# Performance work log

Hardware: AMD Instinct MI355X
Metric: run time of the kernel (lower is better)

## Reference

```python
import jax, jax.numpy as jnp
import numpy as np

EPS = 1e-5  # BatchNorm eps (eval mode, running stats mean=0, var=1)
BN_SCALE = 1.0 / np.sqrt(1.0 + EPS)


def setup_inputs() -> dict:
    key = jax.random.key(0)
    ks = jax.random.split(key, 5)
    N, T, C, V, K = 64, 300, 64, 25, 3
    x = jax.random.normal(ks[0], (N, T, C, V), dtype=jnp.float32)
    # G: Linear(T -> 2T, no bias), Linear(2T -> K, no bias)
    g_w1 = jax.random.normal(ks[1], (2 * T, T), dtype=jnp.float32) * (1.0 / np.sqrt(T))
    g_w2 = jax.random.normal(ks[2], (K, 2 * T), dtype=jnp.float32) * (1.0 / np.sqrt(2 * T))
    # L: Conv1d(C -> C//4, K, pad=K//2, no bias), Conv1d(C//4 -> C, 1, no bias)
    l_w1 = jax.random.normal(ks[3], (C // 4, C, K), dtype=jnp.float32) * (1.0 / np.sqrt(C * K))
    l_w2 = jax.random.normal(ks[4], (C, C // 4), dtype=jnp.float32) * (1.0 / np.sqrt(C // 4))
    return {"x": x, "g_w1": g_w1, "g_w2": g_w2, "l_w1": l_w1, "l_w2": l_w2}


def reference(x, g_w1, g_w2, l_w1, l_w2):
    # x: [N, T, C, V]; n_segment == T so n_batch == N
    N, T, C, V = x.shape
    K = g_w2.shape[0]
    pad = K // 2
    # new_x: [N, C, T, V]
    new_x = jnp.transpose(x, (0, 2, 1, 3))
    # adaptive avg pool over V -> [N, C, T]
    pooled = jnp.mean(new_x, axis=-1)

    # --- G branch: per-(n,c) temporal kernel of size K ---
    g_in = pooled.reshape(N * C, T)                         # [N*C, T]
    h = jnp.maximum(g_in @ g_w1.T * BN_SCALE, 0.0)          # Linear + BN(eval) + ReLU
    conv_kernel = jax.nn.softmax(h @ g_w2.T, axis=-1)       # [N*C, K]
    conv_kernel = conv_kernel.reshape(N, C, K)

    # --- L branch: local activation over time ---
    z = jax.lax.conv_general_dilated(
        pooled, l_w1, window_strides=(1,), padding=[(pad, pad)],
        dimension_numbers=("NCH", "OIH", "NCH"))              # [N, C//4, T]
    z = jnp.maximum(z * BN_SCALE, 0.0)
    local_act = jax.nn.sigmoid(jnp.einsum("nct,oc->not", z, l_w2))  # [N, C, T]

    new_x = new_x * local_act[..., None]                    # [N, C, T, V]

    # --- per-(n,c) depthwise temporal conv (groups = N*C) ---
    xpad = jnp.pad(new_x, ((0, 0), (0, 0), (pad, pad), (0, 0)))
    windows = jnp.stack([xpad[:, :, k:k + T, :] for k in range(K)], axis=-1)  # [N,C,T,V,K]
    out = jnp.einsum("nctvk,nck->nctv", windows, conv_kernel)

    return jnp.transpose(out, (0, 2, 1, 3))                 # [N, T, C, V]
```

## Files before the change

### kernel.cpp

```cpp
#include <hip/hip_runtime.h>
#include <math.h>

#define BN_SCALE_F 0.99999500003749969f


__global__ __launch_bounds__(256) void pool_prep_kernel(const float* __restrict__ x,
                                                        const float* __restrict__ g_w1,
                                                        const float* __restrict__ l_w1,
                                                        float* __restrict__ pooled,
                                                        float* __restrict__ w1p,
                                                        float* __restrict__ lw1r) {
  __shared__ float buf[6400];
  int bid = blockIdx.x;
  if (bid < 4800) {
    const float4* src = (const float4*)(x + (size_t)bid * 6400);
    float4* b4 = (float4*)buf;
    for (int i = threadIdx.x; i < 1600; i += 256) b4[i] = src[i];
    __syncthreads();
    int wave = threadIdx.x >> 6;
    int c = threadIdx.x & 63;
    int nt = bid * 4 + wave;
    int n = nt / 300, t = nt - n * 300;
    const float* p = buf + wave * 1600 + c * 25;
    float s = 0.f;
#pragma unroll
    for (int v = 0; v < 25; ++v) s += p[v];
    pooled[((size_t)(n * 64 + c)) * 300 + t] = s * 0.04f;
  } else if (bid < 4850) {
    int b = bid - 4800;
    float* tile = buf;
    int tj = b % 10, tk = b / 10;
    int j0 = tj * 64, k0 = tk * 64;
    for (int it = 0; it < 16; ++it) {
      int i = threadIdx.x + it * 256;
      int jj = i >> 6, kk = i & 63;
      int j = j0 + jj, k = k0 + kk;
      tile[jj * 65 + kk] = (j < 600 && k < 300) ? g_w1[(size_t)j * 300 + k] : 0.f;
    }
    __syncthreads();
    for (int it = 0; it < 16; ++it) {
      int jloc = threadIdx.x >> 2;
      int kkm = threadIdx.x & 3;
      int kloc = it * 4 + kkm;
      int j = j0 + jloc, k = k0 + kloc;
      if (j < 600 && k < 300) {
        w1p[(size_t)(k >> 2) * 2400 + (size_t)j * 4 + (k & 3)] = tile[jloc * 65 + kloc];
      }
    }
  } else {
    for (int i = threadIdx.x; i < 3072; i += 256) {
      int o = i / 192;
      int rem = i - o * 192;
      int c = rem / 3;
      int k = rem - c * 3;
      lw1r[c * 48 + o * 3 + k] = l_w1[i];
    }
  }
}

union GLSmem {
  struct {
    float rows[8][300];
    float wsum[5][24];
  } g;
  struct {
    float p[64][80];
    float z[75][20];
  } l;
};

__global__ __launch_bounds__(320) void gl_kernel(const float* __restrict__ pooled,
                                                 const float* __restrict__ w1p,
                                                 const float* __restrict__ g_w2,
                                                 const float* __restrict__ lw1r,
                                                 const float* __restrict__ l_w2,
                                                 float* __restrict__ kern,
                                                 float* __restrict__ la) {
  __shared__ GLSmem sm;
  int bid = blockIdx.x;
  int tid = threadIdx.x;
  if (bid < 512) {
    int r0 = bid * 8;
    {
      const float4* src = (const float4*)(pooled + (size_t)r0 * 300);
      float4* dst = (float4*)&sm.g.rows[0][0];
      for (int i = tid; i < 600; i += 320) dst[i] = src[i];
    }
    __syncthreads();

    int j1 = tid;
    int j2 = tid + 320;
    bool has2 = (j2 < 600);
    int j2c = has2 ? j2 : j1;
    const float4* wp = (const float4*)w1p;

    float acc1[8], acc2[8];
#pragma unroll
    for (int r = 0; r < 8; ++r) { acc1[r] = 0.f; acc2[r] = 0.f; }

    float4 wa = wp[j1];
    float4 wb = wp[j2c];
    for (int k4 = 0; k4 < 75; ++k4) {
      float4 wan, wbn;
      if (k4 < 74) {
        wan = wp[(size_t)(k4 + 1) * 600 + j1];
        wbn = wp[(size_t)(k4 + 1) * 600 + j2c];
      } else {
        wan = wa;
        wbn = wb;
      }
#pragma unroll
      for (int r = 0; r < 8; ++r) {
        float4 rv = *(const float4*)(&sm.g.rows[r][k4 * 4]);
        acc1[r] = fmaf(rv.x, wa.x, acc1[r]);
        acc1[r] = fmaf(rv.y, wa.y, acc1[r]);
        acc1[r] = fmaf(rv.z, wa.z, acc1[r]);
        acc1[r] = fmaf(rv.w, wa.w, acc1[r]);
        acc2[r] = fmaf(rv.x, wb.x, acc2[r]);
        acc2[r] = fmaf(rv.y, wb.y, acc2[r]);
        acc2[r] = fmaf(rv.z, wb.z, acc2[r]);
        acc2[r] = fmaf(rv.w, wb.w, acc2[r]);
      }
      wa = wan;
      wb = wbn;
    }

    float w2a0 = g_w2[j1], w2a1 = g_w2[600 + j1], w2a2 = g_w2[1200 + j1];
    float w2b0 = g_w2[j2c], w2b1 = g_w2[600 + j2c], w2b2 = g_w2[1200 + j2c];

    float lacc[24];
#pragma unroll
    for (int r = 0; r < 8; ++r) {
      float h1 = fmaxf(acc1[r] * BN_SCALE_F, 0.f);
      float h2 = has2 ? fmaxf(acc2[r] * BN_SCALE_F, 0.f) : 0.f;
      lacc[r * 3 + 0] = fmaf(h1, w2a0, h2 * w2b0);
      lacc[r * 3 + 1] = fmaf(h1, w2a1, h2 * w2b1);
      lacc[r * 3 + 2] = fmaf(h1, w2a2, h2 * w2b2);
    }

#pragma unroll
    for (int off = 1; off < 64; off <<= 1) {
#pragma unroll
      for (int i = 0; i < 24; ++i) lacc[i] += __shfl_xor(lacc[i], off, 64);
    }
    int wave = tid >> 6;
    int lane = tid & 63;
    if (lane == 0) {
#pragma unroll
      for (int i = 0; i < 24; ++i) sm.g.wsum[wave][i] = lacc[i];
    }
    __syncthreads();
    if (wave == 0) {
      float s = 0.f;
      if (lane < 24) {
#pragma unroll
        for (int w = 0; w < 5; ++w) s += sm.g.wsum[w][lane];
      }
      float a = __shfl(s, lane * 3 + 0, 64);
      float b = __shfl(s, lane * 3 + 1, 64);
      float c = __shfl(s, lane * 3 + 2, 64);
      if (lane < 8) {
        float m = fmaxf(a, fmaxf(b, c));
        float ea = expf(a - m), eb = expf(b - m), ec = expf(c - m);
        float inv = 1.f / (ea + eb + ec);
        size_t o = (size_t)(r0 + lane) * 3;
        kern[o] = ea * inv;
        kern[o + 1] = eb * inv;
        kern[o + 2] = ec * inv;
      }
    }
  } else {
    int bid2 = bid - 512;
    int n = bid2 >> 2;
    int tc = bid2 & 3;
    int t0 = tc * 75;
    for (int i = tid; i < 64 * 77; i += 320) {
      int c = i / 77, tt = i - c * 77;
      int gt = t0 - 1 + tt;
      sm.l.p[c][tt] = (gt >= 0 && gt < 300) ? pooled[(size_t)(n * 64 + c) * 300 + gt] : 0.f;
    }
    __syncthreads();
    {
      int og = tid / 80;
      int tl = tid - og * 80;
      if (tl < 75) {
        float acc[4] = {0.f, 0.f, 0.f, 0.f};
        for (int c = 0; c < 64; ++c) {
          const float* wr = lw1r + c * 48 + og * 12;
          float pk0 = sm.l.p[c][tl];
          float pk1 = sm.l.p[c][tl + 1];
          float pk2 = sm.l.p[c][tl + 2];
#pragma unroll
          for (int oi = 0; oi < 4; ++oi) {
            acc[oi] = fmaf(wr[oi * 3 + 0], pk0, acc[oi]);
            acc[oi] = fmaf(wr[oi * 3 + 1], pk1, acc[oi]);
            acc[oi] = fmaf(wr[oi * 3 + 2], pk2, acc[oi]);
          }
        }
        float4 zv;
        zv.x = fmaxf(acc[0] * BN_SCALE_F, 0.f);
        zv.y = fmaxf(acc[1] * BN_SCALE_F, 0.f);
        zv.z = fmaxf(acc[2] * BN_SCALE_F, 0.f);
        zv.w = fmaxf(acc[3] * BN_SCALE_F, 0.f);
        *(float4*)(&sm.l.z[tl][og * 4]) = zv;
      }
    }
    __syncthreads();
    {
      int c = tid / 5;
      int ts = tid - c * 5;
      const float4* w2v = (const float4*)(l_w2 + c * 16);
      float4 wA = w2v[0], wB = w2v[1], wC = w2v[2], wD = w2v[3];
      float* outp = la + (size_t)(n * 64 + c) * 300 + t0;
      for (int it = 0; it < 15; ++it) {
        int tl = ts + it * 5;
        const float4* zv = (const float4*)(&sm.l.z[tl][0]);
        float4 zA = zv[0], zB = zv[1], zC = zv[2], zD = zv[3];
        float s = zA.x * wA.x + zA.y * wA.y + zA.z * wA.z + zA.w * wA.w;
        s += zB.x * wB.x + zB.y * wB.y + zB.z * wB.z + zB.w * wB.w;
        s += zC.x * wC.x + zC.y * wC.y + zC.z * wC.z + zC.w * wC.w;
        s += zD.x * wD.x + zD.y * wD.y + zD.z * wD.z + zD.w * wD.w;
        outp[tl] = 1.f / (1.f + expf(-s));
      }
    }
  }
}

__global__ __launch_bounds__(256) void tam_final_kernel(const float* __restrict__ x,
                                                        const float* __restrict__ la,
                                                        const float* __restrict__ kern,
                                                        float* __restrict__ out) {
  int bid = blockIdx.x;
  int n = bid >> 4;
  int rem = bid & 15;
  int tch = rem >> 1;
  int half = rem & 1;
  int cv4 = half * 256 + threadIdx.x;
  if (cv4 >= 400) return;
  int e0 = cv4 * 4;
  int c0 = e0 / 25;
  int c3 = (e0 + 3) / 25;
  bool s1 = ((e0 + 1) / 25) != c0;
  bool s2 = ((e0 + 2) / 25) != c0;
  bool s3 = (c3 != c0);
  const float* lap0 = la + (size_t)(n * 64 + c0) * 300;
  const float* lap1 = la + (size_t)(n * 64 + c3) * 300;
  const float* kp0 = kern + (size_t)(n * 64 + c0) * 3;
  const float* kp1 = kern + (size_t)(n * 64 + c3) * 3;
  float k00 = kp0[0], k01 = kp0[1], k02 = kp0[2];
  float k10 = kp1[0], k11 = kp1[1], k12 = kp1[2];
  float4 K0 = {k00, s1 ? k10 : k00, s2 ? k10 : k00, s3 ? k10 : k00};
  float4 K1 = {k01, s1 ? k11 : k01, s2 ? k11 : k01, s3 ? k11 : k01};
  float4 K2 = {k02, s1 ? k12 : k02, s2 ? k12 : k02, s3 ? k12 : k02};

  const float4* xp = (const float4*)(x + (size_t)n * 480000) + cv4;
  float4* op = (float4*)(out + (size_t)n * 480000) + cv4;

  int t0 = tch * 38;
  int tend = t0 + 38;
  if (tend > 300) tend = 300;

#define LAMUL(dst, t)                                        \
  {                                                          \
    float l0 = lap0[(t)];                                    \
    float l1 = lap1[(t)];                                    \
    float4 xv = xp[(size_t)(t) * 400];                       \
    dst.x = xv.x * l0;                                       \
    dst.y = xv.y * (s1 ? l1 : l0);                           \
    dst.z = xv.z * (s2 ? l1 : l0);                           \
    dst.w = xv.w * (s3 ? l1 : l0);                           \
  }

  float4 am, ac, an;
  if (t0 > 0) {
    LAMUL(am, t0 - 1);
  } else {
    am = {0.f, 0.f, 0.f, 0.f};
  }
  LAMUL(ac, t0);
  for (int t = t0; t < tend; ++t) {
    if (t + 1 < 300) {
      LAMUL(an, t + 1);
    } else {
      an = {0.f, 0.f, 0.f, 0.f};
    }
    float4 o;
    o.x = fmaf(am.x, K0.x, fmaf(ac.x, K1.x, an.x * K2.x));
    o.y = fmaf(am.y, K0.y, fmaf(ac.y, K1.y, an.y * K2.y));
    o.z = fmaf(am.z, K0.z, fmaf(ac.z, K1.z, an.z * K2.z));
    o.w = fmaf(am.w, K0.w, fmaf(ac.w, K1.w, an.w * K2.w));
    op[(size_t)t * 400] = o;
    am = ac;
    ac = an;
  }
#undef LAMUL
}

extern "C" void kernel_launch(void* const* d_in, const int* in_sizes, int n_in,
                              void* d_out, int out_size, void* d_ws, size_t ws_size,
                              hipStream_t stream) {
  const float* x = (const float*)d_in[0];
  const float* g_w1 = (const float*)d_in[1];
  const float* g_w2 = (const float*)d_in[2];
  const float* l_w1 = (const float*)d_in[3];
  const float* l_w2 = (const float*)d_in[4];
  float* out = (float*)d_out;
  float* ws = (float*)d_ws;
  float* pooled = ws;
  float* kern = ws + 1228800;
  float* lact = ws + 1228800 + 12288;
  float* w1p = ws + 1228800 + 12288 + 1228800;
  float* lw1r = w1p + 180000;

  hipLaunchKernelGGL(pool_prep_kernel, dim3(4851), dim3(256), 0, stream, x, g_w1, l_w1,
                     pooled, w1p, lw1r);
  hipLaunchKernelGGL(gl_kernel, dim3(768), dim3(320), 0, stream, pooled, w1p, g_w2,
                     lw1r, l_w2, kern, lact);
  hipLaunchKernelGGL(tam_final_kernel, dim3(1024), dim3(256), 0, stream, x, lact, kern, out);
}
```

Before: 122.2 us.

## Register-tile G-branch GEMM with 4 outputs per thread and LDS-staged second layer

Reworks the G-branch first Linear so 150 threads each compute 4 hidden units times 8 rows, raising register reuse of the LDS row reads. Hidden activations are written to shared memory, and the second Linear is computed per (row,k) logit by one wave reduction each, replacing the 24-value butterfly shuffle reduction across all threads. The cost is that only 150 of 320 threads do the main GEMM, a larger shared-memory footprint, and an extra barrier.

```diff
diff --git a/kernel.cpp b/kernel.cpp
--- a/kernel.cpp
+++ b/kernel.cpp
@@ -61,7 +61,8 @@
 union GLSmem {
   struct {
     float rows[8][300];
-    float wsum[5][24];
+    float hbuf[8][600];
+    float logits[24];
   } g;
   struct {
     float p[64][80];
@@ -88,86 +89,68 @@
     }
     __syncthreads();
 
-    int j1 = tid;
-    int j2 = tid + 320;
-    bool has2 = (j2 < 600);
-    int j2c = has2 ? j2 : j1;
-    const float4* wp = (const float4*)w1p;
-
-    float acc1[8], acc2[8];
-#pragma unroll
-    for (int r = 0; r < 8; ++r) { acc1[r] = 0.f; acc2[r] = 0.f; }
-
-    float4 wa = wp[j1];
-    float4 wb = wp[j2c];
-    for (int k4 = 0; k4 < 75; ++k4) {
-      float4 wan, wbn;
-      if (k4 < 74) {
-        wan = wp[(size_t)(k4 + 1) * 600 + j1];
-        wbn = wp[(size_t)(k4 + 1) * 600 + j2c];
-      } else {
-        wan = wa;
-        wbn = wb;
-      }
-#pragma unroll
-      for (int r = 0; r < 8; ++r) {
-        float4 rv = *(const float4*)(&sm.g.rows[r][k4 * 4]);
-        acc1[r] = fmaf(rv.x, wa.x, acc1[r]);
-        acc1[r] = fmaf(rv.y, wa.y, acc1[r]);
-        acc1[r] = fmaf(rv.z, wa.z, acc1[r]);
-        acc1[r] = fmaf(rv.w, wa.w, acc1[r]);
-        acc2[r] = fmaf(rv.x, wb.x, acc2[r]);
-        acc2[r] = fmaf(rv.y, wb.y, acc2[r]);
-        acc2[r] = fmaf(rv.z, wb.z, acc2[r]);
-        acc2[r] = fmaf(rv.w, wb.w, acc2[r]);
-      }
-      wa = wan;
-      wb = wbn;
-    }
-
-    float w2a0 = g_w2[j1], w2a1 = g_w2[600 + j1], w2a2 = g_w2[1200 + j1];
-    float w2b0 = g_w2[j2c], w2b1 = g_w2[600 + j2c], w2b2 = g_w2[1200 + j2c];
-
-    float lacc[24];
-#pragma unroll
-    for (int r = 0; r < 8; ++r) {
-      float h1 = fmaxf(acc1[r] * BN_SCALE_F, 0.f);
-      float h2 = has2 ? fmaxf(acc2[r] * BN_SCALE_F, 0.f) : 0.f;
-      lacc[r * 3 + 0] = fmaf(h1, w2a0, h2 * w2b0);
-      lacc[r * 3 + 1] = fmaf(h1, w2a1, h2 * w2b1);
-      lacc[r * 3 + 2] = fmaf(h1, w2a2, h2 * w2b2);
-    }
-
-#pragma unroll
-    for (int off = 1; off < 64; off <<= 1) {
-#pragma unroll
-      for (int i = 0; i < 24; ++i) lacc[i] += __shfl_xor(lacc[i], off, 64);
-    }
-    int wave = tid >> 6;
-    int lane = tid & 63;
-    if (lane == 0) {
-#pragma unroll
-      for (int i = 0; i < 24; ++i) sm.g.wsum[wave][i] = lacc[i];
-    }
-    __syncthreads();
-    if (wave == 0) {
+    float acc[4][8];
+#pragma unroll
+    for (int s = 0; s < 4; ++s)
+#pragma unroll
+      for (int r = 0; r < 8; ++r) acc[s][r] = 0.f;
+
+    if (tid < 150) {
+      const float4* wp = (const float4*)w1p;
+      float4 wv[4], wn[4];
+#pragma unroll
+      for (int s = 0; s < 4; ++s) wv[s] = wp[tid + 150 * s];
+      for (int k4 = 0; k4 < 75; ++k4) {
+        int nk = (k4 < 74) ? k4 + 1 : 74;
+#pragma unroll
+        for (int s = 0; s < 4; ++s) wn[s] = wp[(size_t)nk * 600 + tid + 150 * s];
+#pragma unroll
+        for (int r = 0; r < 8; ++r) {
+          float4 rv = *(const float4*)(&sm.g.rows[r][k4 * 4]);
+#pragma unroll
+          for (int s = 0; s < 4; ++s) {
+            acc[s][r] = fmaf(rv.x, wv[s].x, acc[s][r]);
+            acc[s][r] = fmaf(rv.y, wv[s].y, acc[s][r]);
+            acc[s][r] = fmaf(rv.z, wv[s].z, acc[s][r]);
+            acc[s][r] = fmaf(rv.w, wv[s].w, acc[s][r]);
+          }
+        }
+#pragma unroll
+        for (int s = 0; s < 4; ++s) wv[s] = wn[s];
+      }
+#pragma unroll
+      for (int s = 0; s < 4; ++s)
+#pragma unroll
+        for (int r = 0; r < 8; ++r)
+          sm.g.hbuf[r][tid + 150 * s] = fmaxf(acc[s][r] * BN_SCALE_F, 0.f);
+    }
+    __syncthreads();
+
+    int wave = tid >> 6, lane = tid & 63;
+    for (int o = wave; o < 24; o += 5) {
+      int r = o / 3, k = o - r * 3;
       float s = 0.f;
-      if (lane < 24) {
-#pragma unroll
-        for (int w = 0; w < 5; ++w) s += sm.g.wsum[w][lane];
-      }
-      float a = __shfl(s, lane * 3 + 0, 64);
-      float b = __shfl(s, lane * 3 + 1, 64);
-      float c = __shfl(s, lane * 3 + 2, 64);
-      if (lane < 8) {
-        float m = fmaxf(a, fmaxf(b, c));
-        float ea = expf(a - m), eb = expf(b - m), ec = expf(c - m);
-        float inv = 1.f / (ea + eb + ec);
-        size_t o = (size_t)(r0 + lane) * 3;
-        kern[o] = ea * inv;
-        kern[o + 1] = eb * inv;
-        kern[o + 2] = ec * inv;
-      }
+#pragma unroll
+      for (int q = 0; q < 10; ++q) {
+        int jj = lane + q * 64;
+        if (jj < 600) s = fmaf(sm.g.hbuf[r][jj], g_w2[k * 600 + jj], s);
+      }
+#pragma unroll
+      for (int off = 1; off < 64; off <<= 1) s += __shfl_xor(s, off, 64);
+      if (lane == 0) sm.g.logits[o] = s;
+    }
+    __syncthreads();
+    if (tid < 8) {
+      float a = sm.g.logits[tid * 3 + 0];
+      float b = sm.g.logits[tid * 3 + 1];
+      float c = sm.g.logits[tid * 3 + 2];
+      float m = fmaxf(a, fmaxf(b, c));
+      float ea = expf(a - m), eb = expf(b - m), ec = expf(c - m);
+      float inv = 1.f / (ea + eb + ec);
+      size_t o = (size_t)(r0 + tid) * 3;
+      kern[o] = ea * inv;
+      kern[o + 1] = eb * inv;
+      kern[o + 2] = ec * inv;
     }
   } else {
     int bid2 = bid - 512;
```

New measurement: 133.1 us. +8.9%, slower.
